# Kernel optimization log

Measured on AMD Instinct MI355X. Metric: run time of the kernel, lower is better.

## Reference

```python
import jax, jax.numpy as jnp
import numpy as np

EMBED_DIM = 1024
NUM_HEADS = 16
DEPTH = EMBED_DIM // NUM_HEADS
SCALE_FACTOR = 0.5
SEQ = 2048
BATCH = 2


def setup_inputs() -> dict:
    key = jax.random.key(0)
    ks = jax.random.split(key, 6)
    x = jax.random.normal(ks[0], (SEQ, BATCH, EMBED_DIM), dtype=jnp.float32)
    attn_mask = jnp.zeros((SEQ, SEQ), dtype=jnp.float32)
    key_padding_mask = jnp.zeros((BATCH, SEQ), dtype=bool)
    # Linear params (torch convention: y = x @ W.T + b)
    s_in = 1.0 / np.sqrt(EMBED_DIM)
    qkv_w = jax.random.uniform(ks[1], (3 * EMBED_DIM, EMBED_DIM), jnp.float32, -s_in, s_in)
    qkv_b = jax.random.uniform(ks[2], (3 * EMBED_DIM,), jnp.float32, -s_in, s_in)
    out_w = jax.random.uniform(ks[3], (EMBED_DIM, EMBED_DIM), jnp.float32, -s_in, s_in)
    out_b = jax.random.uniform(ks[4], (EMBED_DIM,), jnp.float32, -s_in, s_in)
    return {"x": x, "attn_mask": attn_mask, "key_padding_mask": key_padding_mask,
            "qkv_w": qkv_w, "qkv_b": qkv_b, "out_w": out_w, "out_b": out_b}


def reference(x, attn_mask, key_padding_mask, qkv_w, qkv_b, out_w, out_b):
    # x: [S, B, E] -> [B, S, E]
    xb = jnp.transpose(x, (1, 0, 2))
    B, S, E = xb.shape
    qkv = xb @ qkv_w.T + qkv_b                       # [B, S, 3E]
    q, k, v = jnp.split(qkv, 3, axis=2)
    def split_heads(t):                              # [B, S, E] -> [B, H, S, d]
        return jnp.transpose(t.reshape(B, S, NUM_HEADS, DEPTH), (0, 2, 1, 3))
    q, k, v = split_heads(q), split_heads(k), split_heads(v)
    scores = jnp.einsum('bhqd,bhkd->bhqk', q, k) / (DEPTH ** SCALE_FACTOR)
    scores = jnp.where(key_padding_mask[:, None, None, :], -jnp.inf, scores)
    scores = scores + attn_mask[None, None, :, :]
    attn = jax.nn.softmax(scores, axis=-1)           # [B, H, S, S] (dropout p=0)
    wa = jnp.einsum('bhqk,bhkd->bhqd', attn, v)      # [B, H, S, d]
    wa = jnp.transpose(wa, (0, 2, 1, 3)).reshape(B, S, E)
    out = wa @ out_w.T + out_b                       # [B, S, E]
    out = jnp.transpose(out, (1, 0, 2))              # [S, B, E]
    attn_mean = jnp.mean(attn, axis=1)               # [B, S, S]
    return out, attn_mean
```

## Files before the change

### kernel.cpp

```cpp
#include <hip/hip_runtime.h>
#include <hip/hip_bf16.h>


#define Sq 2048
#define Bb 2
#define Ee 1024
#define Hh 16
#define Dd 64
#define LOG2E 1.4426950408889634f
#define QSCALE 0.18033688011112042f

typedef __attribute__((ext_vector_type(8))) short bhalf8;
typedef __attribute__((ext_vector_type(4))) float f32x4;

__device__ __forceinline__ void gld16(const __hip_bfloat16* g, __hip_bfloat16* l) {
    __builtin_amdgcn_global_load_lds(
        (const __attribute__((address_space(1))) unsigned int*)g,
        (__attribute__((address_space(3))) unsigned int*)l, 16, 0, 0);
}

__device__ __forceinline__ int pkbf(float a, float b) {
    int r;
    asm("v_cvt_pk_bf16_f32 %0, %1, %2" : "=v"(r) : "v"(a), "v"(b));
    return r;
}

__device__ __forceinline__ int tile_off(int s) {
    return ((s >> 2) & 1) * 2048 + (s >> 7) * 512 + (s & 3) * 128 + ((s >> 3) & 15) * 8;
}

__device__ __forceinline__ int swz(int t) {
    return (t & ~63) | ((t & 7) << 3) | ((t >> 3) & 7);
}

__device__ __forceinline__ int kperm(int p) {
    return (p & 3) | (((p >> 5) & 1) << 2) | ((p & 12) << 1) | (((p >> 4) & 1) << 5);
}

__global__ __launch_bounds__(256) void prep_k(
    const float* __restrict__ x, const float* __restrict__ am,
    const unsigned int* __restrict__ kpm32,
    const float* __restrict__ qkv_w, const float* __restrict__ out_w,
    __hip_bfloat16* __restrict__ xb, __hip_bfloat16* __restrict__ qwb,
    __hip_bfloat16* __restrict__ owb, unsigned int* __restrict__ flag)
{
    const long i = (long)blockIdx.x*256 + threadIdx.x;
    if (i < 1048576) {
        float4 v = ((const float4*)am)[i];
        bool nz = (v.x != 0.f) | (v.y != 0.f) | (v.z != 0.f) | (v.w != 0.f);
        if (i < 1024) nz |= (kpm32[i] != 0u);
        if (__ballot(nz)) { if ((threadIdx.x & 63) == 0) atomicOr(flag, 1u); }
    } else if (i < 2097152) {
        const long j = i - 1048576;
        const int m = (int)(j >> 8), e4 = (int)(j & 255);
        const int b = m >> 11, s = m & 2047;
        float4 v = ((const float4*)x)[(size_t)(s*Bb + b)*256 + e4];
        uint2 o;
        o.x = (unsigned)pkbf(v.x, v.y);
        o.y = (unsigned)pkbf(v.z, v.w);
        ((uint2*)xb)[(size_t)m*256 + e4] = o;
    } else if (i < 2883584) {
        const long j = i - 2097152;
        float4 v = ((const float4*)qkv_w)[j];
        uint2 o;
        o.x = (unsigned)pkbf(v.x, v.y);
        o.y = (unsigned)pkbf(v.z, v.w);
        ((uint2*)qwb)[j] = o;
    } else if (i < 3145728) {
        const long j = i - 2883584;
        float4 v = ((const float4*)out_w)[j];
        uint2 o;
        o.x = (unsigned)pkbf(v.x, v.y);
        o.y = (unsigned)pkbf(v.z, v.w);
        ((uint2*)owb)[j] = o;
    }
}

__global__ __launch_bounds__(256) void gemm_qkv(
    const __hip_bfloat16* __restrict__ A, const __hip_bfloat16* __restrict__ Bw,
    const float* __restrict__ bias,
    __hip_bfloat16* __restrict__ Qp, __hip_bfloat16* __restrict__ Kp,
    __hip_bfloat16* __restrict__ Vt)
{
    __shared__ __align__(16) __hip_bfloat16 As[128*32];
    __shared__ __align__(16) __hip_bfloat16 Bs[128*32];
    const int t = threadIdx.x;
    const int l = t & 63, lm = l & 15, quad = l >> 4;
    const int w = t >> 6;
    const int mw = (w & 1)*64, nw = (w >> 1)*64;
    const int m0 = blockIdx.y*128, n0 = blockIdx.x*128;

    const int srow = t >> 2;
    const int scol = (t & 3)*8;
    const __hip_bfloat16* ag = A  + (size_t)(m0 + srow)*1024 + scol;
    const __hip_bfloat16* bg = Bw + (size_t)(n0 + srow)*1024 + scol;
    __hip_bfloat16* al = As + t*8;
    __hip_bfloat16* bl = Bs + t*8;

    f32x4 acc[4][4] = {};
    for (int k0 = 0; k0 < 1024; k0 += 32) {
        __syncthreads();
        gld16(ag + k0, al);
        gld16(ag + (size_t)64*1024 + k0, al + 2048);
        gld16(bg + k0, bl);
        gld16(bg + (size_t)64*1024 + k0, bl + 2048);
        __syncthreads();
        bhalf8 af[4], bf[4];
#pragma unroll
        for (int i = 0; i < 4; i++) {
            af[i] = *(const bhalf8*)&As[(mw + i*16 + lm)*32 + quad*8];
            bf[i] = *(const bhalf8*)&Bs[(nw + i*16 + lm)*32 + quad*8];
        }
#pragma unroll
        for (int mf = 0; mf < 4; mf++)
#pragma unroll
            for (int nf = 0; nf < 4; nf++)
                acc[mf][nf] = __builtin_amdgcn_mfma_f32_16x16x32_bf16(af[mf], bf[nf], acc[mf][nf], 0,0,0);
    }
#pragma unroll
    for (int nf = 0; nf < 4; nf++) {
        const int n = n0 + nw + nf*16 + lm;
        const float bz = bias[n];
        const int which = n >> 10, hh = (n >> 6) & 15, dd = n & 63;
#pragma unroll
        for (int mf = 0; mf < 4; mf++)
#pragma unroll
            for (int r = 0; r < 4; r++) {
                const int m = m0 + mw + mf*16 + quad*4 + r;
                const int b2 = m >> 11, s2 = m & 2047;
                const float vf = acc[mf][nf][r] + bz;
                if (which == 0)
                    Qp[((size_t)(b2*Hh + hh)*Sq + s2)*Dd + dd] = __float2bfloat16(vf * QSCALE);
                else if (which == 1)
                    Kp[((size_t)(b2*Hh + hh)*Sq + s2)*Dd + dd] = __float2bfloat16(vf);
                else
                    Vt[((size_t)(b2*Hh + hh)*Dd + dd)*Sq + s2] = __float2bfloat16(vf);
            }
    }
}

__global__ __launch_bounds__(256, 4) void attn_mfma(
    const __hip_bfloat16* __restrict__ Qp, const __hip_bfloat16* __restrict__ Kp,
    const __hip_bfloat16* __restrict__ Vt,
    const float* __restrict__ am, const unsigned char* __restrict__ kpm,
    const unsigned int* __restrict__ flag,
    __hip_bfloat16* __restrict__ wa, float* __restrict__ rlbuf)
{
    __shared__ __align__(16) __hip_bfloat16 Ks[4096];
    __shared__ __align__(16) __hip_bfloat16 Vs[4096];
    const int t = threadIdx.x;
    const int w = t >> 6, l = t & 63, lm = l & 15, quad = l >> 4;
    const int blk = blockIdx.x;
    const int xcd = blk & 7;
    const int qt  = (blk >> 3) & 31;
    const int grp = blk >> 8;
    const int bh  = grp*8 + xcd;
    const int b   = bh >> 4, h = bh & 15;
    const int q   = qt*64 + w*16 + lm;
    const bool masked = (flag[0] != 0u);

    const __hip_bfloat16* qbase = Qp + (size_t)bh*Sq*Dd;
    const __hip_bfloat16* kbase = Kp + (size_t)bh*Sq*Dd;
    const __hip_bfloat16* vbase = Vt + (size_t)bh*Dd*Sq;

    bhalf8 bq[2];
    bq[0] = *(const bhalf8*)(qbase + (size_t)q*Dd + quad*8);
    bq[1] = *(const bhalf8*)(qbase + (size_t)q*Dd + quad*8 + 32);

    f32x4 o[4] = {};
    float lsum = 0.f;

    const int g0 = swz(t), g1 = g0 + 256;
    const int off0 = tile_off(g0), off1 = tile_off(g1);
    const int krow0 = kperm(g0 >> 3);
    const int krow1 = kperm(g1 >> 3);
    const int kcol  = (g0 & 7)*8;
    const int vrow0 = g0 >> 3, vrow1 = g1 >> 3;

    uint4 kreg0 = *(const uint4*)(kbase + (size_t)krow0*Dd + kcol);
    uint4 kreg1 = *(const uint4*)(kbase + (size_t)krow1*Dd + kcol);
    uint4 vreg0 = *(const uint4*)(vbase + (size_t)vrow0*Sq + kcol);
    uint4 vreg1 = *(const uint4*)(vbase + (size_t)vrow1*Sq + kcol);

    for (int kt = 0; kt < 32; kt++) {
        __syncthreads();
        *(uint4*)&Ks[off0] = kreg0;
        *(uint4*)&Ks[off1] = kreg1;
        *(uint4*)&Vs[off0] = vreg0;
        *(uint4*)&Vs[off1] = vreg1;
        if (kt < 31) {
            const int kn = (kt + 1)*64;
            kreg0 = *(const uint4*)(kbase + (size_t)(kn + krow0)*Dd + kcol);
            kreg1 = *(const uint4*)(kbase + (size_t)(kn + krow1)*Dd + kcol);
            vreg0 = *(const uint4*)(vbase + (size_t)vrow0*Sq + kn + kcol);
            vreg1 = *(const uint4*)(vbase + (size_t)vrow1*Sq + kn + kcol);
        }
        __syncthreads();

        const int k0 = kt*64;
        f32x4 s[4] = {};
#pragma unroll
        for (int f = 0; f < 2; f++) {
            bhalf8 ak[4];
#pragma unroll
            for (int j = 0; j < 4; j++)
                ak[j] = *(const bhalf8*)&Ks[f*2048 + j*512 + l*8];
#pragma unroll
            for (int j = 0; j < 4; j++)
                s[j] = __builtin_amdgcn_mfma_f32_16x16x32_bf16(ak[j], bq[f], s[j], 0,0,0);
        }

        int pk[4][2];
#pragma unroll
        for (int j = 0; j < 4; j++) {
            float p[4];
#pragma unroll
            for (int r = 0; r < 4; r++) {
                float sv = s[j][r];
                if (masked) {
                    const int key = k0 + 32*(j & 1) + 8*quad + 4*(j >> 1) + r;
                    const float km = kpm[b*Sq + key] ? -1e30f : 0.0f;
                    sv += (am[(size_t)q*Sq + key] + km) * LOG2E;
                }
                p[r] = exp2f(sv);
            }
            lsum += (p[0]+p[1]) + (p[2]+p[3]);
            pk[j][0] = pkbf(p[0], p[1]);
            pk[j][1] = pkbf(p[2], p[3]);
        }

#pragma unroll
        for (int ks = 0; ks < 2; ks++) {
            union { int i[4]; bhalf8 v; } bp;
            bp.i[0] = pk[ks][0];
            bp.i[1] = pk[ks][1];
            bp.i[2] = pk[ks + 2][0];
            bp.i[3] = pk[ks + 2][1];
            bhalf8 av[4];
#pragma unroll
            for (int nd = 0; nd < 4; nd++)
                av[nd] = *(const bhalf8*)&Vs[ks*2048 + nd*512 + l*8];
#pragma unroll
            for (int nd = 0; nd < 4; nd++)
                o[nd] = __builtin_amdgcn_mfma_f32_16x16x32_bf16(av[nd], bp.v, o[nd], 0,0,0);
        }
    }

    lsum += __shfl_xor(lsum, 16, 64);
    lsum += __shfl_xor(lsum, 32, 64);
    const float rl = 1.0f / lsum;
    if (quad == 0) rlbuf[(size_t)bh*Sq + q] = rl * 0.0625f;

#pragma unroll
    for (int nd = 0; nd < 4; nd++) {
        uint2 ou;
        ou.x = (unsigned)pkbf(o[nd][0] * rl, o[nd][1] * rl);
        ou.y = (unsigned)pkbf(o[nd][2] * rl, o[nd][3] * rl);
        *(uint2*)(wa + ((size_t)b*Sq + q)*Ee + h*Dd + nd*16 + quad*4) = ou;
    }
}

__global__ __launch_bounds__(256) void tail_k(
    const __hip_bfloat16* __restrict__ Qp, const __hip_bfloat16* __restrict__ Kp,
    const float* __restrict__ am, const unsigned char* __restrict__ kpm,
    const unsigned int* __restrict__ flag,
    const float* __restrict__ rlbuf, float* __restrict__ attn_mean,
    const __hip_bfloat16* __restrict__ A, const __hip_bfloat16* __restrict__ Bw,
    const float* __restrict__ bias, float* __restrict__ outp)
{
    __shared__ __align__(16) __hip_bfloat16 sh[8192];
    const int t = threadIdx.x;
    const int l = t & 63, lm = l & 15, quad = l >> 4;
    const int w = t >> 6;

    if (blockIdx.x < 256) {
        __hip_bfloat16* As = sh;
        __hip_bfloat16* Bs = sh + 4096;
        const int mw = (w & 1)*64, nw = (w >> 1)*64;
        const int n0 = (blockIdx.x & 7)*128, m0 = (blockIdx.x >> 3)*128;

        const int srow = t >> 2;
        const int scol = (t & 3)*8;
        const __hip_bfloat16* ag = A  + (size_t)(m0 + srow)*1024 + scol;
        const __hip_bfloat16* bg = Bw + (size_t)(n0 + srow)*1024 + scol;
        __hip_bfloat16* al = As + t*8;
        __hip_bfloat16* bl = Bs + t*8;

        f32x4 acc[4][4] = {};
        for (int k0 = 0; k0 < 1024; k0 += 32) {
            __syncthreads();
            gld16(ag + k0, al);
            gld16(ag + (size_t)64*1024 + k0, al + 2048);
            gld16(bg + k0, bl);
            gld16(bg + (size_t)64*1024 + k0, bl + 2048);
            __syncthreads();
            bhalf8 af[4], bf[4];
#pragma unroll
            for (int i = 0; i < 4; i++) {
                af[i] = *(const bhalf8*)&As[(mw + i*16 + lm)*32 + quad*8];
                bf[i] = *(const bhalf8*)&Bs[(nw + i*16 + lm)*32 + quad*8];
            }
#pragma unroll
            for (int mf = 0; mf < 4; mf++)
#pragma unroll
                for (int nf = 0; nf < 4; nf++)
                    acc[mf][nf] = __builtin_amdgcn_mfma_f32_16x16x32_bf16(af[mf], bf[nf], acc[mf][nf], 0,0,0);
        }
#pragma unroll
        for (int nf = 0; nf < 4; nf++) {
            const int n = n0 + nw + nf*16 + lm;
            const float bz = bias[n];
#pragma unroll
            for (int mf = 0; mf < 4; mf++)
#pragma unroll
                for (int r = 0; r < 4; r++) {
                    const int m = m0 + mw + mf*16 + quad*4 + r;
                    const int b2 = m >> 11, s2 = m & 2047;
                    outp[((size_t)s2*Bb + b2)*Ee + n] = acc[mf][nf][r] + bz;
                }
        }
        return;
    }

    __hip_bfloat16 (*Ks)[4096] = (__hip_bfloat16(*)[4096])sh;
    const int blk = blockIdx.x - 256;
    const int q0idx = (blk & 7) | (((blk >> 8) & 1) << 3);
    const int kc    = ((blk >> 3) & 31) * 64;
    const int b     = (blk >> 9) & 1;
    const int q0    = q0idx * 128;
    const bool masked = (flag[0] != 0u);

    const int g0 = swz(t), g1 = g0 + 256;
    const int off0 = tile_off(g0), off1 = tile_off(g1);
    const int qa = q0 + w*32;

    float macc[2][4][4] = {};
    uint4 kr0, kr1;

    {
        const __hip_bfloat16* kg = Kp + ((size_t)(b*Hh)*Sq + kc)*Dd;
        uint4 a0 = *(const uint4*)(kg + (size_t)g0*8);
        uint4 a1 = *(const uint4*)(kg + (size_t)g1*8);
        *(uint4*)&Ks[0][off0] = a0;
        *(uint4*)&Ks[0][off1] = a1;
        const __hip_bfloat16* kg1 = kg + (size_t)Sq*Dd;
        kr0 = *(const uint4*)(kg1 + (size_t)g0*8);
        kr1 = *(const uint4*)(kg1 + (size_t)g1*8);
    }

    for (int h = 0; h < Hh; h++) {
        __syncthreads();
        if (h < Hh - 1) {
            *(uint4*)&Ks[(h + 1) & 1][off0] = kr0;
            *(uint4*)&Ks[(h + 1) & 1][off1] = kr1;
            if (h < Hh - 2) {
                const __hip_bfloat16* kn = Kp + ((size_t)(b*Hh + h + 2)*Sq + kc)*Dd;
                kr0 = *(const uint4*)(kn + (size_t)g0*8);
                kr1 = *(const uint4*)(kn + (size_t)g1*8);
            }
        }

        const size_t base = (size_t)(b*Hh + h)*Sq;
        const __hip_bfloat16* Kc = Ks[h & 1];
#pragma unroll
        for (int su = 0; su < 2; su++) {
            const int qrow = qa + su*16;
            const __hip_bfloat16* qg = Qp + (base + qrow + lm)*Dd + quad*8;
            f32x4 s[4] = {};
#pragma unroll
            for (int f = 0; f < 2; f++) {
                bhalf8 aq = *(const bhalf8*)(qg + f*32);
#pragma unroll
                for (int j = 0; j < 4; j++) {
                    bhalf8 bk = *(const bhalf8*)&Kc[f*2048 + j*512 + l*8];
                    s[j] = __builtin_amdgcn_mfma_f32_16x16x32_bf16(aq, bk, s[j], 0,0,0);
                }
            }
            const f32x4 rl4 = *(const f32x4*)(rlbuf + base + qrow + quad*4);
#pragma unroll
            for (int j = 0; j < 4; j++)
#pragma unroll
                for (int r = 0; r < 4; r++) {
                    float sv = s[j][r];
                    if (masked) {
                        const int key = kc + j*16 + lm;
                        const float km = kpm[b*Sq + key] ? -1e30f : 0.0f;
                        sv += (am[(size_t)(qrow + quad*4 + r)*Sq + key] + km) * LOG2E;
                    }
                    macc[su][j][r] += exp2f(sv) * rl4[r];
                }
        }
    }

#pragma unroll
    for (int su = 0; su < 2; su++)
#pragma unroll
        for (int j = 0; j < 4; j++)
#pragma unroll
            for (int r = 0; r < 4; r++)
                attn_mean[((size_t)b*Sq + qa + su*16 + quad*4 + r)*Sq + kc + j*16 + lm] =
                    macc[su][j][r];
}

extern "C" void kernel_launch(void* const* d_in, const int* in_sizes, int n_in,
                              void* d_out, int out_size, void* d_ws, size_t ws_size,
                              hipStream_t stream) {
    const float*         x         = (const float*)d_in[0];
    const float*         attn_mask = (const float*)d_in[1];
    const unsigned char* kpm       = (const unsigned char*)d_in[2];
    const float*         qkv_w     = (const float*)d_in[3];
    const float*         qkv_b     = (const float*)d_in[4];
    const float*         out_w     = (const float*)d_in[5];
    const float*         out_b     = (const float*)d_in[6];

    float* outp      = (float*)d_out;
    float* attn_mean = outp + 4194304;

    __hip_bfloat16* xb  = (__hip_bfloat16*)d_ws;
    __hip_bfloat16* qwb = xb  + 4194304;
    __hip_bfloat16* owb = qwb + 3145728;
    __hip_bfloat16* Qp  = owb + 1048576;
    __hip_bfloat16* Kp  = Qp  + 4194304;
    __hip_bfloat16* Vt  = Kp  + 4194304;
    __hip_bfloat16* wab = Vt  + 4194304;
    float* rlbuf        = (float*)(wab + 4194304);
    unsigned int* flag  = (unsigned int*)(rlbuf + 65536);

    hipMemsetAsync(flag, 0, sizeof(unsigned int), stream);
    prep_k<<<12288, 256, 0, stream>>>(x, attn_mask, (const unsigned int*)kpm,
                                      qkv_w, out_w, xb, qwb, owb, flag);
    gemm_qkv<<<dim3(24, 32), 256, 0, stream>>>(xb, qwb, qkv_b, Qp, Kp, Vt);
    attn_mfma<<<dim3(1024), 256, 0, stream>>>(Qp, Kp, Vt, attn_mask, kpm, flag, wab, rlbuf);
    tail_k<<<dim3(1280), 256, 0, stream>>>(Qp, Kp, attn_mask, kpm, flag, rlbuf, attn_mean,
                                           wab, owb, out_b, outp);
}
```

Before: 308.1 us.

## Split fused tail kernel and software-pipeline Q and rowsum loads across heads

Splits the combined out-projection GEMM plus attention-mean kernel into two separate launches, so neither carries the branchy, heterogeneous-block structure. Inside the attention-mean kernel, the Q fragments and reciprocal row sums for the next head are prefetched into registers while the current head is computed, using ping-pong buffers and a two-way unrolled head loop. This hides global-load latency in the head loop. In exchange it adds a kernel launch, loses the overlap the fused kernel had between GEMM blocks and mean blocks, and raises register pressure.

After: 350.7 us. 13.8% more time.

```diff
diff --git a/kernel.cpp b/kernel.cpp
--- a/kernel.cpp
+++ b/kernel.cpp
@@ -260,70 +260,16 @@
     }
 }
 
-__global__ __launch_bounds__(256) void tail_k(
+__global__ __launch_bounds__(256) void attn_mean_k(
     const __hip_bfloat16* __restrict__ Qp, const __hip_bfloat16* __restrict__ Kp,
     const float* __restrict__ am, const unsigned char* __restrict__ kpm,
     const unsigned int* __restrict__ flag,
-    const float* __restrict__ rlbuf, float* __restrict__ attn_mean,
-    const __hip_bfloat16* __restrict__ A, const __hip_bfloat16* __restrict__ Bw,
-    const float* __restrict__ bias, float* __restrict__ outp)
+    const float* __restrict__ rlbuf, float* __restrict__ attn_mean)
 {
-    __shared__ __align__(16) __hip_bfloat16 sh[8192];
+    __shared__ __align__(16) __hip_bfloat16 Ks[2][4096];
     const int t = threadIdx.x;
-    const int l = t & 63, lm = l & 15, quad = l >> 4;
-    const int w = t >> 6;
-
-    if (blockIdx.x < 256) {
-        __hip_bfloat16* As = sh;
-        __hip_bfloat16* Bs = sh + 4096;
-        const int mw = (w & 1)*64, nw = (w >> 1)*64;
-        const int n0 = (blockIdx.x & 7)*128, m0 = (blockIdx.x >> 3)*128;
-
-        const int srow = t >> 2;
-        const int scol = (t & 3)*8;
-        const __hip_bfloat16* ag = A  + (size_t)(m0 + srow)*1024 + scol;
-        const __hip_bfloat16* bg = Bw + (size_t)(n0 + srow)*1024 + scol;
-        __hip_bfloat16* al = As + t*8;
-        __hip_bfloat16* bl = Bs + t*8;
-
-        f32x4 acc[4][4] = {};
-        for (int k0 = 0; k0 < 1024; k0 += 32) {
-            __syncthreads();
-            gld16(ag + k0, al);
-            gld16(ag + (size_t)64*1024 + k0, al + 2048);
-            gld16(bg + k0, bl);
-            gld16(bg + (size_t)64*1024 + k0, bl + 2048);
-            __syncthreads();
-            bhalf8 af[4], bf[4];
-#pragma unroll
-            for (int i = 0; i < 4; i++) {
-                af[i] = *(const bhalf8*)&As[(mw + i*16 + lm)*32 + quad*8];
-                bf[i] = *(const bhalf8*)&Bs[(nw + i*16 + lm)*32 + quad*8];
-            }
-#pragma unroll
-            for (int mf = 0; mf < 4; mf++)
-#pragma unroll
-                for (int nf = 0; nf < 4; nf++)
-                    acc[mf][nf] = __builtin_amdgcn_mfma_f32_16x16x32_bf16(af[mf], bf[nf], acc[mf][nf], 0,0,0);
-        }
-#pragma unroll
-        for (int nf = 0; nf < 4; nf++) {
-            const int n = n0 + nw + nf*16 + lm;
-            const float bz = bias[n];
-#pragma unroll
-            for (int mf = 0; mf < 4; mf++)
-#pragma unroll
-                for (int r = 0; r < 4; r++) {
-                    const int m = m0 + mw + mf*16 + quad*4 + r;
-                    const int b2 = m >> 11, s2 = m & 2047;
-                    outp[((size_t)s2*Bb + b2)*Ee + n] = acc[mf][nf][r] + bz;
-                }
-        }
-        return;
-    }
-
-    __hip_bfloat16 (*Ks)[4096] = (__hip_bfloat16(*)[4096])sh;
-    const int blk = blockIdx.x - 256;
+    const int w = t >> 6, l = t & 63, lm = l & 15, quad = l >> 4;
+    const int blk = blockIdx.x;
     const int q0idx = (blk & 7) | (((blk >> 8) & 1) << 3);
     const int kc    = ((blk >> 3) & 31) * 64;
     const int b     = (blk >> 9) & 1;
@@ -336,6 +282,8 @@
 
     float macc[2][4][4] = {};
     uint4 kr0, kr1;
+    bhalf8 aqA[2][2], aqB[2][2];
+    f32x4  rlA[2],    rlB[2];
 
     {
         const __hip_bfloat16* kg = Kp + ((size_t)(b*Hh)*Sq + kc)*Dd;
@@ -346,9 +294,18 @@
         const __hip_bfloat16* kg1 = kg + (size_t)Sq*Dd;
         kr0 = *(const uint4*)(kg1 + (size_t)g0*8);
         kr1 = *(const uint4*)(kg1 + (size_t)g1*8);
-    }
-
-    for (int h = 0; h < Hh; h++) {
+        const size_t b0 = (size_t)(b*Hh)*Sq;
+#pragma unroll
+        for (int su = 0; su < 2; su++) {
+            const __hip_bfloat16* qg = Qp + (b0 + qa + su*16 + lm)*Dd + quad*8;
+            aqA[su][0] = *(const bhalf8*)(qg);
+            aqA[su][1] = *(const bhalf8*)(qg + 32);
+            rlA[su] = *(const f32x4*)(rlbuf + b0 + qa + su*16 + quad*4);
+        }
+    }
+
+    auto body = [&](int h, bhalf8 (&aqc)[2][2], f32x4 (&rlc)[2],
+                           bhalf8 (&aqn)[2][2], f32x4 (&rln)[2]) {
         __syncthreads();
         if (h < Hh - 1) {
             *(uint4*)&Ks[(h + 1) & 1][off0] = kr0;
@@ -358,25 +315,29 @@
                 kr0 = *(const uint4*)(kn + (size_t)g0*8);
                 kr1 = *(const uint4*)(kn + (size_t)g1*8);
             }
-        }
-
-        const size_t base = (size_t)(b*Hh + h)*Sq;
+            const size_t bn = (size_t)(b*Hh + h + 1)*Sq;
+#pragma unroll
+            for (int su = 0; su < 2; su++) {
+                const __hip_bfloat16* qg = Qp + (bn + qa + su*16 + lm)*Dd + quad*8;
+                aqn[su][0] = *(const bhalf8*)(qg);
+                aqn[su][1] = *(const bhalf8*)(qg + 32);
+                rln[su] = *(const f32x4*)(rlbuf + bn + qa + su*16 + quad*4);
+            }
+        }
+
         const __hip_bfloat16* Kc = Ks[h & 1];
 #pragma unroll
         for (int su = 0; su < 2; su++) {
             const int qrow = qa + su*16;
-            const __hip_bfloat16* qg = Qp + (base + qrow + lm)*Dd + quad*8;
             f32x4 s[4] = {};
 #pragma unroll
             for (int f = 0; f < 2; f++) {
-                bhalf8 aq = *(const bhalf8*)(qg + f*32);
 #pragma unroll
                 for (int j = 0; j < 4; j++) {
                     bhalf8 bk = *(const bhalf8*)&Kc[f*2048 + j*512 + l*8];
-                    s[j] = __builtin_amdgcn_mfma_f32_16x16x32_bf16(aq, bk, s[j], 0,0,0);
+                    s[j] = __builtin_amdgcn_mfma_f32_16x16x32_bf16(aqc[su][f], bk, s[j], 0,0,0);
                 }
             }
-            const f32x4 rl4 = *(const f32x4*)(rlbuf + base + qrow + quad*4);
 #pragma unroll
             for (int j = 0; j < 4; j++)
 #pragma unroll
@@ -387,9 +348,14 @@
                         const float km = kpm[b*Sq + key] ? -1e30f : 0.0f;
                         sv += (am[(size_t)(qrow + quad*4 + r)*Sq + key] + km) * LOG2E;
                     }
-                    macc[su][j][r] += exp2f(sv) * rl4[r];
+                    macc[su][j][r] += exp2f(sv) * rlc[su][r];
                 }
         }
+    };
+
+    for (int h = 0; h < Hh; h += 2) {
+        body(h,     aqA, rlA, aqB, rlB);
+        body(h + 1, aqB, rlB, aqA, rlA);
     }
 
 #pragma unroll
@@ -400,6 +366,60 @@
             for (int r = 0; r < 4; r++)
                 attn_mean[((size_t)b*Sq + qa + su*16 + quad*4 + r)*Sq + kc + j*16 + lm] =
                     macc[su][j][r];
+}
+
+__global__ __launch_bounds__(256) void gemm_out(
+    const __hip_bfloat16* __restrict__ A, const __hip_bfloat16* __restrict__ Bw,
+    const float* __restrict__ bias, float* __restrict__ outp)
+{
+    __shared__ __align__(16) __hip_bfloat16 As[128*32];
+    __shared__ __align__(16) __hip_bfloat16 Bs[128*32];
+    const int t = threadIdx.x;
+    const int l = t & 63, lm = l & 15, quad = l >> 4;
+    const int w = t >> 6;
+    const int mw = (w & 1)*64, nw = (w >> 1)*64;
+    const int m0 = blockIdx.y*128, n0 = blockIdx.x*128;
+
+    const int srow = t >> 2;
+    const int scol = (t & 3)*8;
+    const __hip_bfloat16* ag = A  + (size_t)(m0 + srow)*1024 + scol;
+    const __hip_bfloat16* bg = Bw + (size_t)(n0 + srow)*1024 + scol;
+    __hip_bfloat16* al = As + t*8;
+    __hip_bfloat16* bl = Bs + t*8;
+
+    f32x4 acc[4][4] = {};
+    for (int k0 = 0; k0 < 1024; k0 += 32) {
+        __syncthreads();
+        gld16(ag + k0, al);
+        gld16(ag + (size_t)64*1024 + k0, al + 2048);
+        gld16(bg + k0, bl);
+        gld16(bg + (size_t)64*1024 + k0, bl + 2048);
+        __syncthreads();
+        bhalf8 af[4], bf[4];
+#pragma unroll
+        for (int i = 0; i < 4; i++) {
+            af[i] = *(const bhalf8*)&As[(mw + i*16 + lm)*32 + quad*8];
+            bf[i] = *(const bhalf8*)&Bs[(nw + i*16 + lm)*32 + quad*8];
+        }
+#pragma unroll
+        for (int mf = 0; mf < 4; mf++)
+#pragma unroll
+            for (int nf = 0; nf < 4; nf++)
+                acc[mf][nf] = __builtin_amdgcn_mfma_f32_16x16x32_bf16(af[mf], bf[nf], acc[mf][nf], 0,0,0);
+    }
+#pragma unroll
+    for (int nf = 0; nf < 4; nf++) {
+        const int n = n0 + nw + nf*16 + lm;
+        const float bz = bias[n];
+#pragma unroll
+        for (int mf = 0; mf < 4; mf++)
+#pragma unroll
+            for (int r = 0; r < 4; r++) {
+                const int m = m0 + mw + mf*16 + quad*4 + r;
+                const int b2 = m >> 11, s2 = m & 2047;
+                outp[((size_t)s2*Bb + b2)*Ee + n] = acc[mf][nf][r] + bz;
+            }
+    }
 }
 
 extern "C" void kernel_launch(void* const* d_in, const int* in_sizes, int n_in,
@@ -431,6 +451,6 @@
                                       qkv_w, out_w, xb, qwb, owb, flag);
     gemm_qkv<<<dim3(24, 32), 256, 0, stream>>>(xb, qwb, qkv_b, Qp, Kp, Vt);
     attn_mfma<<<dim3(1024), 256, 0, stream>>>(Qp, Kp, Vt, attn_mask, kpm, flag, wab, rlbuf);
-    tail_k<<<dim3(1280), 256, 0, stream>>>(Qp, Kp, attn_mask, kpm, flag, rlbuf, attn_mean,
-                                           wab, owb, out_b, outp);
-}
+    attn_mean_k<<<dim3(1024), 256, 0, stream>>>(Qp, Kp, attn_mask, kpm, flag, rlbuf, attn_mean);
+    gemm_out<<<dim3(8, 32), 256, 0, stream>>>(wab, owb, out_b, outp);
+}
```
